# Kernel tuning notes

Measured on AMD Instinct MI355X. Metric: run time of the kernel, lower is better.

The kernel has to match this reference:

```python
import jax, jax.numpy as jnp
import numpy as np
import math

B, S, H = 4, 2048, 1024


def setup_inputs() -> dict:
    key = jax.random.key(0)
    ks = jax.random.split(key, 9)
    scale = 1.0 / math.sqrt(H)
    x = jax.random.normal(ks[0], (B, S, H), dtype=jnp.float32)
    attention_mask = jax.random.randint(ks[1], (B, S, S), 0, 2, dtype=jnp.int32)
    Wq = jax.random.uniform(ks[2], (H, H), jnp.float32, -scale, scale)
    bq = jax.random.uniform(ks[3], (H,), jnp.float32, -scale, scale)
    Wk = jax.random.uniform(ks[4], (H, H), jnp.float32, -scale, scale)
    bk = jax.random.uniform(ks[5], (H,), jnp.float32, -scale, scale)
    Wv = jax.random.uniform(ks[6], (H, H), jnp.float32, -scale, scale)
    bv = jax.random.uniform(ks[7], (H,), jnp.float32, -scale, scale)
    return {"x": x, "attention_mask": attention_mask,
            "Wq": Wq, "bq": bq, "Wk": Wk, "bk": bk, "Wv": Wv, "bv": bv}


def reference(x, attention_mask, Wq, bq, Wk, bk, Wv, bv):
    # q/k/v projections (torch Linear: x @ W.T + b)
    q = jnp.einsum('bsh,oh->bso', x, Wq) + bq
    k = jnp.einsum('bsh,oh->bso', x, Wk) + bk
    v = jnp.einsum('bsh,oh->bso', x, Wv) + bv
    # raw scores [B,S,S]
    scores = jnp.einsum('bqh,bkh->bqk', q, k)
    # NOTE: faithful to original - mask fill happens BEFORE the 1/sqrt(H) scaling
    scores = jnp.where(attention_mask == 0, jnp.float32(-1e9), scores)
    attn = jax.nn.softmax(scores / math.sqrt(H), axis=-1)
    # dropout p=0.0 (eval mode) -> identity
    return jnp.einsum('bqk,bkh->bqh', attn, v)
```

## Files before the change

kernel.cpp:

```cpp
#include <hip/hip_runtime.h>

#define B_ 4
#define S_ 2048
#define H_ 1024

typedef __bf16 bf16x8 __attribute__((ext_vector_type(8)));
typedef float  f32x4  __attribute__((ext_vector_type(4)));

__device__ __forceinline__ unsigned short f2bf(float f) {
  unsigned u = __float_as_uint(f);
  u += 0x7FFF + ((u >> 16) & 1);
  return (unsigned short)(u >> 16);
}

__global__ void cvt_kernel(const float* __restrict__ in,
                           unsigned short* __restrict__ out, int n4) {
  int i = blockIdx.x * blockDim.x + threadIdx.x;
  if (i >= n4) return;
  const float4 v = reinterpret_cast<const float4*>(in)[i];
  ushort4 o;
  o.x = f2bf(v.x); o.y = f2bf(v.y); o.z = f2bf(v.z); o.w = f2bf(v.w);
  reinterpret_cast<ushort4*>(out)[i] = o;
}

__device__ __forceinline__ void stage_tile(const unsigned short* __restrict__ g,
                                           long row0, long ld, long k0,
                                           char* s, int t) {
  int wave = t >> 6;
#pragma unroll
  for (int i = 0; i < 4; ++i) {
    int ci  = i * 256 + t;
    int off = ci << 4;
    int r   = off >> 7;
    int o   = off & 127;
    int osw = o ^ ((r & 7) << 4);
    const char* gp = reinterpret_cast<const char*>(g + (row0 + r) * ld + k0) + osw;
    char* lp = s + ((i * 256 + wave * 64) << 4);
    __builtin_amdgcn_global_load_lds((const __attribute__((address_space(1))) void*)gp,
                                     (__attribute__((address_space(3))) void*)lp,
                                     16, 0, 0);
  }
}

template <int KSTEPS>
__device__ __forceinline__ void gemm_loop(const unsigned short* __restrict__ A, long ldA, long m0,
                                          const unsigned short* __restrict__ Bm, long ldB, long n0,
                                          char* smem, f32x4 acc[4][4]) {
  const int t    = threadIdx.x;
  const int lane = t & 63;
  const int wr   = (t >> 7) & 1;
  const int wc   = (t >> 6) & 1;
  char* sA = smem;
  char* sB = smem + 16384;
  for (int kt = 0; kt < KSTEPS; ++kt) {
    __syncthreads();
    stage_tile(A,  m0, ldA, (long)kt * 64, sA, t);
    stage_tile(Bm, n0, ldB, (long)kt * 64, sB, t);
    __syncthreads();
#pragma unroll
    for (int ks = 0; ks < 2; ++ks) {
      bf16x8 af[4], bfr[4];
      const int kb = ks * 64 + (lane >> 4) * 16;
#pragma unroll
      for (int mf = 0; mf < 4; ++mf) {
        int row = wr * 64 + mf * 16 + (lane & 15);
        af[mf] = *reinterpret_cast<const bf16x8*>(sA + row * 128 + (kb ^ ((row & 7) << 4)));
      }
#pragma unroll
      for (int nf = 0; nf < 4; ++nf) {
        int row = wc * 64 + nf * 16 + (lane & 15);
        bfr[nf] = *reinterpret_cast<const bf16x8*>(sB + row * 128 + (kb ^ ((row & 7) << 4)));
      }
#pragma unroll
      for (int mf = 0; mf < 4; ++mf)
#pragma unroll
        for (int nf = 0; nf < 4; ++nf)
          acc[mf][nf] = __builtin_amdgcn_mfma_f32_16x16x32_bf16(af[mf], bfr[nf], acc[mf][nf], 0, 0, 0);
    }
  }
}

__global__ __launch_bounds__(256) void qkv_kernel(
    const unsigned short* __restrict__ x, const unsigned short* __restrict__ W3,
    const float* __restrict__ bq, const float* __restrict__ bk, const float* __restrict__ bv,
    unsigned short* __restrict__ Q, unsigned short* __restrict__ K, unsigned short* __restrict__ V) {
  __shared__ char smem[32768];
  const int z = blockIdx.z;
  const unsigned short* W = W3 + (size_t)z * (H_ * H_);
  const float* bias = (z == 0) ? bq : (z == 1) ? bk : bv;
  unsigned short* out = (z == 0) ? Q : (z == 1) ? K : V;
  const long m0 = (long)blockIdx.y * 128, n0 = (long)blockIdx.x * 128;
  f32x4 acc[4][4] = {};
  gemm_loop<H_ / 64>(x, H_, m0, W, H_, n0, smem, acc);
  const int lane = threadIdx.x & 63;
  const int wr = (threadIdx.x >> 7) & 1, wc = (threadIdx.x >> 6) & 1;
#pragma unroll
  for (int nf = 0; nf < 4; ++nf) {
    long col = n0 + wc * 64 + nf * 16 + (lane & 15);
    float bb = bias[col];
#pragma unroll
    for (int mf = 0; mf < 4; ++mf)
#pragma unroll
      for (int r = 0; r < 4; ++r) {
        long row = m0 + wr * 64 + mf * 16 + (lane >> 4) * 4 + r;
        out[row * H_ + col] = f2bf(acc[mf][nf][r] + bb);
      }
  }
}

__global__ void vtrans_kernel(const unsigned short* __restrict__ V,
                              unsigned short* __restrict__ VT) {
  __shared__ unsigned short tile[64][66];
  const int b = blockIdx.z;
  const int c0 = blockIdx.x * 64;
  const int r0 = blockIdx.y * 64;
  const int tx = threadIdx.x, ty = threadIdx.y;
  const unsigned short* Vb = V + (size_t)b * S_ * H_;
  unsigned short* VTb = VT + (size_t)b * H_ * S_;
#pragma unroll
  for (int i = 0; i < 16; ++i) {
    int r = ty * 16 + i;
    tile[r][tx] = Vb[(size_t)(r0 + r) * H_ + c0 + tx];
  }
  __syncthreads();
#pragma unroll
  for (int i = 0; i < 16; ++i) {
    int c = ty * 16 + i;
    VTb[(size_t)(c0 + c) * S_ + r0 + tx] = tile[tx][c];
  }
}

__global__ __launch_bounds__(256) void scores_kernel(
    const unsigned short* __restrict__ Q, const unsigned short* __restrict__ Km,
    const int* __restrict__ mask, unsigned short* __restrict__ P,
    float* __restrict__ rowsum) {
  __shared__ char smem[32768];
  const int b = blockIdx.z;
  const long m0 = (long)blockIdx.y * 128, n0 = (long)blockIdx.x * 128;
  const unsigned short* Qb = Q + (size_t)b * S_ * H_;
  const unsigned short* Kb = Km + (size_t)b * S_ * H_;
  const int* Mb = mask + (size_t)b * S_ * S_;
  unsigned short* Pb = P + (size_t)b * S_ * S_;
  f32x4 acc[4][4] = {};
  gemm_loop<H_ / 64>(Qb, H_, m0, Kb, H_, n0, smem, acc);
  const int lane = threadIdx.x & 63;
  const int wr = (threadIdx.x >> 7) & 1, wc = (threadIdx.x >> 6) & 1;
#pragma unroll
  for (int mf = 0; mf < 4; ++mf) {
#pragma unroll
    for (int r = 0; r < 4; ++r) {
      long row = m0 + wr * 64 + mf * 16 + (lane >> 4) * 4 + r;
      float rs = 0.f;
#pragma unroll
      for (int nf = 0; nf < 4; ++nf) {
        long col = n0 + wc * 64 + nf * 16 + (lane & 15);
        float p = Mb[row * S_ + col] ? __expf(acc[mf][nf][r] * 0.03125f) : 0.f;
        Pb[row * S_ + col] = f2bf(p);
        rs += p;
      }
#pragma unroll
      for (int s = 1; s < 16; s <<= 1) rs += __shfl_xor(rs, s, 64);
      if ((lane & 15) == 0) atomicAdd(&rowsum[(size_t)b * S_ + row], rs);
    }
  }
}

__global__ __launch_bounds__(256) void pv_kernel(
    const unsigned short* __restrict__ P, const unsigned short* __restrict__ VT,
    const float* __restrict__ rowsum, float* __restrict__ out) {
  __shared__ char smem[32768];
  const int b = blockIdx.z;
  const long m0 = (long)blockIdx.y * 128, n0 = (long)blockIdx.x * 128;
  const unsigned short* Pb = P + (size_t)b * S_ * S_;
  const unsigned short* VTb = VT + (size_t)b * H_ * S_;
  f32x4 acc[4][4] = {};
  gemm_loop<S_ / 64>(Pb, S_, m0, VTb, S_, n0, smem, acc);
  const int lane = threadIdx.x & 63;
  const int wr = (threadIdx.x >> 7) & 1, wc = (threadIdx.x >> 6) & 1;
#pragma unroll
  for (int mf = 0; mf < 4; ++mf)
#pragma unroll
    for (int r = 0; r < 4; ++r) {
      long row = m0 + wr * 64 + mf * 16 + (lane >> 4) * 4 + r;
      float inv = 1.f / rowsum[(size_t)b * S_ + row];
#pragma unroll
      for (int nf = 0; nf < 4; ++nf) {
        long col = n0 + wc * 64 + nf * 16 + (lane & 15);
        out[((size_t)b * S_ + row) * H_ + col] = acc[mf][nf][r] * inv;
      }
    }
}

extern "C" void kernel_launch(void* const* d_in, const int* in_sizes, int n_in,
                              void* d_out, int out_size, void* d_ws, size_t ws_size,
                              hipStream_t stream) {
  const float* x   = (const float*)d_in[0];
  const int* mask  = (const int*)d_in[1];
  const float* Wq  = (const float*)d_in[2];
  const float* bq  = (const float*)d_in[3];
  const float* Wk  = (const float*)d_in[4];
  const float* bk  = (const float*)d_in[5];
  const float* Wv  = (const float*)d_in[6];
  const float* bv  = (const float*)d_in[7];
  float* out = (float*)d_out;

  const size_t MS = (size_t)B_ * S_ * H_;
  unsigned short* xb  = (unsigned short*)d_ws;
  unsigned short* W3  = xb + MS;
  unsigned short* Qb  = W3 + (size_t)3 * H_ * H_;
  unsigned short* Kb  = Qb + MS;
  unsigned short* Vb  = Kb + MS;
  unsigned short* VTb = Vb + MS;
  unsigned short* Pb  = VTb + MS;
  float* rowsum = (float*)(Pb + (size_t)B_ * S_ * S_);

  hipMemsetAsync(rowsum, 0, (size_t)B_ * S_ * sizeof(float), stream);

  cvt_kernel<<<(int)(MS / 4 / 256), 256, 0, stream>>>(x, xb, (int)(MS / 4));
  cvt_kernel<<<H_ * H_ / 4 / 256, 256, 0, stream>>>(Wq, W3, H_ * H_ / 4);
  cvt_kernel<<<H_ * H_ / 4 / 256, 256, 0, stream>>>(Wk, W3 + H_ * H_, H_ * H_ / 4);
  cvt_kernel<<<H_ * H_ / 4 / 256, 256, 0, stream>>>(Wv, W3 + 2 * H_ * H_, H_ * H_ / 4);

  qkv_kernel<<<dim3(H_ / 128, (B_ * S_) / 128, 3), 256, 0, stream>>>(
      xb, W3, bq, bk, bv, Qb, Kb, Vb);

  vtrans_kernel<<<dim3(H_ / 64, S_ / 64, B_), dim3(64, 4), 0, stream>>>(Vb, VTb);

  scores_kernel<<<dim3(S_ / 128, S_ / 128, B_), 256, 0, stream>>>(
      Qb, Kb, mask, Pb, rowsum);

  pv_kernel<<<dim3(H_ / 128, S_ / 128, B_), 256, 0, stream>>>(Pb, VTb, rowsum, out);
}
```

Before: 334.6 us.

## Switch GEMMs to 256x256 tiles with double-buffered LDS prefetch pipeline

```diff
diff --git a/kernel.cpp b/kernel.cpp
--- a/kernel.cpp
+++ b/kernel.cpp
@@ -13,97 +13,152 @@
   return (unsigned short)(u >> 16);
 }
 
-__global__ void cvt_kernel(const float* __restrict__ in,
-                           unsigned short* __restrict__ out, int n4) {
+__global__ void cvt_all_kernel(const float* __restrict__ x,
+                               const float* __restrict__ wq,
+                               const float* __restrict__ wk,
+                               const float* __restrict__ wv,
+                               unsigned short* __restrict__ dst) {
   int i = blockIdx.x * blockDim.x + threadIdx.x;
-  if (i >= n4) return;
-  const float4 v = reinterpret_cast<const float4*>(in)[i];
-  ushort4 o;
-  o.x = f2bf(v.x); o.y = f2bf(v.y); o.z = f2bf(v.z); o.w = f2bf(v.w);
-  reinterpret_cast<ushort4*>(out)[i] = o;
-}
-
-__device__ __forceinline__ void stage_tile(const unsigned short* __restrict__ g,
-                                           long row0, long ld, long k0,
-                                           char* s, int t) {
-  int wave = t >> 6;
-#pragma unroll
-  for (int i = 0; i < 4; ++i) {
-    int ci  = i * 256 + t;
-    int off = ci << 4;
-    int r   = off >> 7;
-    int o   = off & 127;
-    int osw = o ^ ((r & 7) << 4);
-    const char* gp = reinterpret_cast<const char*>(g + (row0 + r) * ld + k0) + osw;
-    char* lp = s + ((i * 256 + wave * 64) << 4);
-    __builtin_amdgcn_global_load_lds((const __attribute__((address_space(1))) void*)gp,
-                                     (__attribute__((address_space(3))) void*)lp,
-                                     16, 0, 0);
-  }
-}
-
-template <int KSTEPS>
-__device__ __forceinline__ void gemm_loop(const unsigned short* __restrict__ A, long ldA, long m0,
-                                          const unsigned short* __restrict__ Bm, long ldB, long n0,
-                                          char* smem, f32x4 acc[4][4]) {
-  const int t    = threadIdx.x;
+  const int NX = (B_ * S_ * H_) / 4;
+  const int NW = (H_ * H_) / 4;
+  const float* src; int off;
+  if (i < NX) { src = x; off = i; }
+  else { int j = i - NX; int w = j >> 18; off = j & (NW - 1);
+         src = (w == 0) ? wq : (w == 1) ? wk : wv; }
+  float4 v = reinterpret_cast<const float4*>(src)[off];
+  ushort4 o; o.x = f2bf(v.x); o.y = f2bf(v.y); o.z = f2bf(v.z); o.w = f2bf(v.w);
+  reinterpret_cast<ushort4*>(dst)[i] = o;
+}
+
+
+__device__ __forceinline__ bf16x8 lfrag(const char* base, int row, int kb) {
+  return *reinterpret_cast<const bf16x8*>(base + row * 128 + (kb ^ ((row & 7) << 4)));
+}
+
+__device__ __forceinline__ void stage_q(const unsigned short* __restrict__ g,
+                                        long row0, long ld, int k0e,
+                                        char* sbase, int q, int t) {
+  int row = q * 64 + (t >> 3);
+  int osw = ((t & 7) << 4) ^ ((row & 7) << 4);
+  const char* gp = reinterpret_cast<const char*>(g + (row0 + row) * ld + k0e) + osw;
+  char* lp = sbase + q * 8192 + ((t >> 6) << 10);
+  __builtin_amdgcn_global_load_lds((const __attribute__((address_space(1))) void*)gp,
+                                   (__attribute__((address_space(3))) void*)lp,
+                                   16, 0, 0);
+}
+
+template <int NT>
+__device__ __forceinline__ void gemm8(const unsigned short* __restrict__ A, long ldA, long m0,
+                                      const unsigned short* __restrict__ Bm, long ldB, long n0,
+                                      char* sm, f32x4 acc[8][4]) {
+  const int t = threadIdx.x;
   const int lane = t & 63;
-  const int wr   = (t >> 7) & 1;
-  const int wc   = (t >> 6) & 1;
-  char* sA = smem;
-  char* sB = smem + 16384;
-  for (int kt = 0; kt < KSTEPS; ++kt) {
-    __syncthreads();
-    stage_tile(A,  m0, ldA, (long)kt * 64, sA, t);
-    stage_tile(Bm, n0, ldB, (long)kt * 64, sB, t);
-    __syncthreads();
-#pragma unroll
-    for (int ks = 0; ks < 2; ++ks) {
-      bf16x8 af[4], bfr[4];
-      const int kb = ks * 64 + (lane >> 4) * 16;
-#pragma unroll
-      for (int mf = 0; mf < 4; ++mf) {
-        int row = wr * 64 + mf * 16 + (lane & 15);
-        af[mf] = *reinterpret_cast<const bf16x8*>(sA + row * 128 + (kb ^ ((row & 7) << 4)));
-      }
-#pragma unroll
-      for (int nf = 0; nf < 4; ++nf) {
-        int row = wc * 64 + nf * 16 + (lane & 15);
-        bfr[nf] = *reinterpret_cast<const bf16x8*>(sB + row * 128 + (kb ^ ((row & 7) << 4)));
-      }
-#pragma unroll
-      for (int mf = 0; mf < 4; ++mf)
+  const int wid = t >> 6;
+  const int wr = wid >> 2, wc = wid & 3;
+  const int lrow = lane & 15;
+  const int kb0 = (lane >> 4) * 16;
+  char* sA0 = sm;          char* sB0 = sm + 32768;
+  char* sA1 = sm + 65536;  char* sB1 = sm + 98304;
+
+#pragma unroll
+  for (int q = 0; q < 4; ++q) stage_q(A, m0, ldA, 0, sA0, q, t);
+#pragma unroll
+  for (int q = 0; q < 4; ++q) stage_q(Bm, n0, ldB, 0, sB0, q, t);
+#pragma unroll
+  for (int q = 0; q < 4; ++q) stage_q(Bm, n0, ldB, 64, sB1, q, t);
+  stage_q(A, m0, ldA, 64, sA1, 0, t);
+  stage_q(A, m0, ldA, 64, sA1, 2, t);
+  asm volatile("s_waitcnt vmcnt(6)" ::: "memory");
+  __builtin_amdgcn_s_barrier();
+
+  auto ktile = [&](int kt, char* cA, char* cB, char* nA) {
+    const int k1 = (kt + 1 < NT ? kt + 1 : NT - 1) * 64;
+    const int k2 = (kt + 2 < NT ? kt + 2 : NT - 1) * 64;
+    bf16x8 bfr[4][2], af[2][2];
+#pragma unroll
+    for (int nf = 0; nf < 4; ++nf)
+#pragma unroll
+      for (int ks = 0; ks < 2; ++ks)
+        bfr[nf][ks] = lfrag(cB, wc * 64 + nf * 16 + lrow, ks * 64 + kb0);
+#pragma unroll
+    for (int mf = 0; mf < 2; ++mf)
+#pragma unroll
+      for (int ks = 0; ks < 2; ++ks)
+        af[mf][ks] = lfrag(cA, wr * 128 + mf * 16 + lrow, ks * 64 + kb0);
+    stage_q(A, m0, ldA, k1, nA, 1, t);
+    stage_q(A, m0, ldA, k1, nA, 3, t);
+    __builtin_amdgcn_s_barrier();
+    asm volatile("s_waitcnt lgkmcnt(0)" ::: "memory");
+    __builtin_amdgcn_sched_barrier(0);
+    __builtin_amdgcn_s_setprio(1);
+#pragma unroll
+    for (int mf = 0; mf < 2; ++mf)
+#pragma unroll
+      for (int nf = 0; nf < 4; ++nf)
+#pragma unroll
+        for (int ks = 0; ks < 2; ++ks)
+          acc[mf][nf] = __builtin_amdgcn_mfma_f32_16x16x32_bf16(af[mf][ks], bfr[nf][ks], acc[mf][nf], 0, 0, 0);
+    __builtin_amdgcn_s_setprio(0);
+    __builtin_amdgcn_s_barrier();
+#pragma unroll
+    for (int q = 1; q < 4; ++q) {
+#pragma unroll
+      for (int mf = 0; mf < 2; ++mf)
+#pragma unroll
+        for (int ks = 0; ks < 2; ++ks)
+          af[mf][ks] = lfrag(cA, wr * 128 + q * 32 + mf * 16 + lrow, ks * 64 + kb0);
+      if (q == 1) { stage_q(Bm, n0, ldB, k2, cB, 0, t); stage_q(Bm, n0, ldB, k2, cB, 1, t); }
+      if (q == 2) { stage_q(Bm, n0, ldB, k2, cB, 2, t); stage_q(Bm, n0, ldB, k2, cB, 3, t); }
+      if (q == 3) { stage_q(A, m0, ldA, k2, cA, 0, t); stage_q(A, m0, ldA, k2, cA, 2, t);
+                    asm volatile("s_waitcnt vmcnt(6)" ::: "memory"); }
+      __builtin_amdgcn_s_barrier();
+      asm volatile("s_waitcnt lgkmcnt(0)" ::: "memory");
+      __builtin_amdgcn_sched_barrier(0);
+      __builtin_amdgcn_s_setprio(1);
+#pragma unroll
+      for (int mf = 0; mf < 2; ++mf)
 #pragma unroll
         for (int nf = 0; nf < 4; ++nf)
-          acc[mf][nf] = __builtin_amdgcn_mfma_f32_16x16x32_bf16(af[mf], bfr[nf], acc[mf][nf], 0, 0, 0);
+#pragma unroll
+          for (int ks = 0; ks < 2; ++ks)
+            acc[2 * q + mf][nf] = __builtin_amdgcn_mfma_f32_16x16x32_bf16(af[mf][ks], bfr[nf][ks], acc[2 * q + mf][nf], 0, 0, 0);
+      __builtin_amdgcn_s_setprio(0);
+      __builtin_amdgcn_s_barrier();
     }
-  }
-}
-
-__global__ __launch_bounds__(256) void qkv_kernel(
+  };
+
+#pragma unroll 1
+  for (int kt = 0; kt < NT; kt += 2) {
+    ktile(kt,     sA0, sB0, sA1);
+    ktile(kt + 1, sA1, sB1, sA0);
+  }
+}
+
+__global__ __launch_bounds__(512, 2) void qkv_kernel(
     const unsigned short* __restrict__ x, const unsigned short* __restrict__ W3,
     const float* __restrict__ bq, const float* __restrict__ bk, const float* __restrict__ bv,
     unsigned short* __restrict__ Q, unsigned short* __restrict__ K, unsigned short* __restrict__ V) {
-  __shared__ char smem[32768];
+  extern __shared__ char sm[];
   const int z = blockIdx.z;
   const unsigned short* W = W3 + (size_t)z * (H_ * H_);
   const float* bias = (z == 0) ? bq : (z == 1) ? bk : bv;
   unsigned short* out = (z == 0) ? Q : (z == 1) ? K : V;
-  const long m0 = (long)blockIdx.y * 128, n0 = (long)blockIdx.x * 128;
-  f32x4 acc[4][4] = {};
-  gemm_loop<H_ / 64>(x, H_, m0, W, H_, n0, smem, acc);
+  const long m0 = (long)blockIdx.y * 256, n0 = (long)blockIdx.x * 256;
+  f32x4 acc[8][4] = {};
+  gemm8<H_ / 64>(x, H_, m0, W, H_, n0, sm, acc);
   const int lane = threadIdx.x & 63;
-  const int wr = (threadIdx.x >> 7) & 1, wc = (threadIdx.x >> 6) & 1;
+  const int wid = threadIdx.x >> 6;
+  const int wr = wid >> 2, wc = wid & 3;
 #pragma unroll
   for (int nf = 0; nf < 4; ++nf) {
     long col = n0 + wc * 64 + nf * 16 + (lane & 15);
     float bb = bias[col];
 #pragma unroll
-    for (int mf = 0; mf < 4; ++mf)
+    for (int mq = 0; mq < 8; ++mq)
 #pragma unroll
       for (int r = 0; r < 4; ++r) {
-        long row = m0 + wr * 64 + mf * 16 + (lane >> 4) * 4 + r;
-        out[row * H_ + col] = f2bf(acc[mf][nf][r] + bb);
+        long row = m0 + wr * 128 + mq * 16 + (lane >> 4) * 4 + r;
+        out[row * H_ + col] = f2bf(acc[mq][nf][r] + bb);
       }
   }
 }
@@ -130,31 +185,32 @@
   }
 }
 
-__global__ __launch_bounds__(256) void scores_kernel(
+__global__ __launch_bounds__(512, 2) void scores_kernel(
     const unsigned short* __restrict__ Q, const unsigned short* __restrict__ Km,
     const int* __restrict__ mask, unsigned short* __restrict__ P,
     float* __restrict__ rowsum) {
-  __shared__ char smem[32768];
+  extern __shared__ char sm[];
   const int b = blockIdx.z;
-  const long m0 = (long)blockIdx.y * 128, n0 = (long)blockIdx.x * 128;
+  const long m0 = (long)blockIdx.y * 256, n0 = (long)blockIdx.x * 256;
   const unsigned short* Qb = Q + (size_t)b * S_ * H_;
   const unsigned short* Kb = Km + (size_t)b * S_ * H_;
   const int* Mb = mask + (size_t)b * S_ * S_;
   unsigned short* Pb = P + (size_t)b * S_ * S_;
-  f32x4 acc[4][4] = {};
-  gemm_loop<H_ / 64>(Qb, H_, m0, Kb, H_, n0, smem, acc);
+  f32x4 acc[8][4] = {};
+  gemm8<H_ / 64>(Qb, H_, m0, Kb, H_, n0, sm, acc);
   const int lane = threadIdx.x & 63;
-  const int wr = (threadIdx.x >> 7) & 1, wc = (threadIdx.x >> 6) & 1;
-#pragma unroll
-  for (int mf = 0; mf < 4; ++mf) {
+  const int wid = threadIdx.x >> 6;
+  const int wr = wid >> 2, wc = wid & 3;
+#pragma unroll
+  for (int mq = 0; mq < 8; ++mq) {
 #pragma unroll
     for (int r = 0; r < 4; ++r) {
-      long row = m0 + wr * 64 + mf * 16 + (lane >> 4) * 4 + r;
+      long row = m0 + wr * 128 + mq * 16 + (lane >> 4) * 4 + r;
       float rs = 0.f;
 #pragma unroll
       for (int nf = 0; nf < 4; ++nf) {
         long col = n0 + wc * 64 + nf * 16 + (lane & 15);
-        float p = Mb[row * S_ + col] ? __expf(acc[mf][nf][r] * 0.03125f) : 0.f;
+        float p = Mb[row * S_ + col] ? __expf(acc[mq][nf][r] * 0.03125f) : 0.f;
         Pb[row * S_ + col] = f2bf(p);
         rs += p;
       }
@@ -165,28 +221,29 @@
   }
 }
 
-__global__ __launch_bounds__(256) void pv_kernel(
+__global__ __launch_bounds__(512, 2) void pv_kernel(
     const unsigned short* __restrict__ P, const unsigned short* __restrict__ VT,
     const float* __restrict__ rowsum, float* __restrict__ out) {
-  __shared__ char smem[32768];
+  extern __shared__ char sm[];
   const int b = blockIdx.z;
-  const long m0 = (long)blockIdx.y * 128, n0 = (long)blockIdx.x * 128;
+  const long m0 = (long)blockIdx.y * 256, n0 = (long)blockIdx.x * 256;
   const unsigned short* Pb = P + (size_t)b * S_ * S_;
   const unsigned short* VTb = VT + (size_t)b * H_ * S_;
-  f32x4 acc[4][4] = {};
-  gemm_loop<S_ / 64>(Pb, S_, m0, VTb, S_, n0, smem, acc);
+  f32x4 acc[8][4] = {};
+  gemm8<S_ / 64>(Pb, S_, m0, VTb, S_, n0, sm, acc);
   const int lane = threadIdx.x & 63;
-  const int wr = (threadIdx.x >> 7) & 1, wc = (threadIdx.x >> 6) & 1;
-#pragma unroll
-  for (int mf = 0; mf < 4; ++mf)
+  const int wid = threadIdx.x >> 6;
+  const int wr = wid >> 2, wc = wid & 3;
+#pragma unroll
+  for (int mq = 0; mq < 8; ++mq)
 #pragma unroll
     for (int r = 0; r < 4; ++r) {
-      long row = m0 + wr * 64 + mf * 16 + (lane >> 4) * 4 + r;
+      long row = m0 + wr * 128 + mq * 16 + (lane >> 4) * 4 + r;
       float inv = 1.f / rowsum[(size_t)b * S_ + row];
 #pragma unroll
       for (int nf = 0; nf < 4; ++nf) {
         long col = n0 + wc * 64 + nf * 16 + (lane & 15);
-        out[((size_t)b * S_ + row) * H_ + col] = acc[mf][nf][r] * inv;
+        out[((size_t)b * S_ + row) * H_ + col] = acc[mq][nf][r] * inv;
       }
     }
 }
@@ -214,20 +271,25 @@
   unsigned short* Pb  = VTb + MS;
   float* rowsum = (float*)(Pb + (size_t)B_ * S_ * S_);
 
+  (void)hipFuncSetAttribute(reinterpret_cast<const void*>(qkv_kernel),
+                            hipFuncAttributeMaxDynamicSharedMemorySize, 131072);
+  (void)hipFuncSetAttribute(reinterpret_cast<const void*>(scores_kernel),
+                            hipFuncAttributeMaxDynamicSharedMemorySize, 131072);
+  (void)hipFuncSetAttribute(reinterpret_cast<const void*>(pv_kernel),
+                            hipFuncAttributeMaxDynamicSharedMemorySize, 131072);
+
   hipMemsetAsync(rowsum, 0, (size_t)B_ * S_ * sizeof(float), stream);
 
-  cvt_kernel<<<(int)(MS / 4 / 256), 256, 0, stream>>>(x, xb, (int)(MS / 4));
-  cvt_kernel<<<H_ * H_ / 4 / 256, 256, 0, stream>>>(Wq, W3, H_ * H_ / 4);
-  cvt_kernel<<<H_ * H_ / 4 / 256, 256, 0, stream>>>(Wk, W3 + H_ * H_, H_ * H_ / 4);
-  cvt_kernel<<<H_ * H_ / 4 / 256, 256, 0, stream>>>(Wv, W3 + 2 * H_ * H_, H_ * H_ / 4);
-
-  qkv_kernel<<<dim3(H_ / 128, (B_ * S_) / 128, 3), 256, 0, stream>>>(
+  const int NCVT = (int)(MS / 4) + 3 * (H_ * H_ / 4);
+  cvt_all_kernel<<<NCVT / 256, 256, 0, stream>>>(x, Wq, Wk, Wv, xb);
+
+  qkv_kernel<<<dim3(H_ / 256, (B_ * S_) / 256, 3), 512, 131072, stream>>>(
       xb, W3, bq, bk, bv, Qb, Kb, Vb);
 
   vtrans_kernel<<<dim3(H_ / 64, S_ / 64, B_), dim3(64, 4), 0, stream>>>(Vb, VTb);
 
-  scores_kernel<<<dim3(S_ / 128, S_ / 128, B_), 256, 0, stream>>>(
+  scores_kernel<<<dim3(S_ / 256, S_ / 256, B_), 512, 131072, stream>>>(
       Qb, Kb, mask, Pb, rowsum);
 
-  pv_kernel<<<dim3(H_ / 128, S_ / 128, B_), 256, 0, stream>>>(Pb, VTb, rowsum, out);
-}
+  pv_kernel<<<dim3(H_ / 256, S_ / 256, B_), 512, 131072, stream>>>(Pb, VTb, rowsum, out);
+}
```

Measured after the change: 324.3 us. 1.03x faster.
